# Optimization experiments

Measured on AMD Instinct MI355X. Metric: run time of the kernel, lower is better.

Reference implementation:

```python
import jax, jax.numpy as jnp
import numpy as np

B, T, D, H = 8, 1024, 512, 8
DK = D // H


def setup_inputs() -> dict:
    key = jax.random.key(0)
    ks = jax.random.split(key, 6)
    s = 0.02
    return {
        "inputs": jax.random.normal(ks[0], (B, T, D), jnp.float32),
        "ln1_g": jnp.ones((D,), jnp.float32),
        "ln1_b": jnp.zeros((D,), jnp.float32),
        "ln2_g": jnp.ones((D,), jnp.float32),
        "ln2_b": jnp.zeros((D,), jnp.float32),
        "W_qkv": jax.random.normal(ks[1], (3 * D, D), jnp.float32) * s,
        "W_pos": jax.random.normal(ks[2], (D, D), jnp.float32) * s,
        "W_out": jax.random.normal(ks[3], (D, D), jnp.float32) * s,
        "b_out": jnp.zeros((D,), jnp.float32),
        "pos_bias_u": jax.random.normal(ks[4], (H, DK), jnp.float32) * s,
        "pos_bias_v": jax.random.normal(ks[5], (H, DK), jnp.float32) * s,
    }


def layer_norm(x, g, b, eps=1e-5):
    mu = jnp.mean(x, axis=-1, keepdims=True)
    var = jnp.var(x, axis=-1, keepdims=True)
    return (x - mu) * jax.lax.rsqrt(var + eps) * g + b


def rel_shift(x):
    # x: (b, h, t1, t2); Transformer-XL pad-reshape-slice relative shift
    b, h, t1, t2 = x.shape
    xp = jnp.pad(x, ((0, 0), (0, 0), (0, 0), (1, 0)))  # zero col at front
    xp = xp.reshape(b, h, t2 + 1, t1)[:, :, 1:, :]
    return xp.reshape(b, h, t1, t2)


def reference(inputs, ln1_g, ln1_b, ln2_g, ln2_b, W_qkv, W_pos, W_out, b_out,
              pos_bias_u, pos_bias_v):
    b, t, d = inputs.shape
    # PositionalEmbedding: pos_seq is the literal data values inputs[0,:,0]
    pos_seq = inputs[0, :, 0]
    inv_freq = 1.0 / (10000.0 ** (jnp.arange(0, d, 2, dtype=jnp.float32) / d))
    sin_inp = pos_seq[:, None] * inv_freq[None, :]  # (T, D/2)
    pos_emb = jnp.concatenate([jnp.sin(sin_inp), jnp.cos(sin_inp)], axis=-1)  # (T, D)
    # outer layer norm, then inner layer norm inside forward_qkv
    x = layer_norm(inputs, ln1_g, ln1_b)
    xn = layer_norm(x, ln2_g, ln2_b)
    qkv = xn @ W_qkv.T  # (B, T, 3D)
    q, k, v = jnp.split(qkv, 3, axis=-1)
    q = q.reshape(b, t, H, DK)                       # (B, T, H, DK)
    k = k.reshape(b, t, H, DK).transpose(0, 2, 1, 3)  # (B, H, T, DK)
    v = v.reshape(b, t, H, DK).transpose(0, 2, 1, 3)  # (B, H, T, DK)
    p = (pos_emb @ W_pos.T).reshape(t, H, DK)         # (T, H, DK), pos batch = 1
    qu = (q + pos_bias_u).transpose(0, 2, 1, 3)       # (B, H, T, DK)
    qv = (q + pos_bias_v).transpose(0, 2, 1, 3)
    ac = jnp.einsum('bhqd,bhkd->bhqk', qu, k)
    bd = jnp.einsum('bhqd,khd->bhqk', qv, p)
    bd = rel_shift(bd)
    scores = (ac + bd) / jnp.sqrt(jnp.float32(DK))
    attn = jax.nn.softmax(scores, axis=-1)
    out = jnp.einsum('bhqk,bhkd->bqhd', attn, v).reshape(b, t, d)
    return out @ W_out.T + b_out
```

## Files before the change

kernel.cpp:

```cpp
#include <hip/hip_runtime.h>
#include <stdint.h>

#define B_ 8
#define T_ 1024
#define D_ 512
#define H_ 8
#define DK_ 64
#define M_ (B_*T_)

#define PREP_CAST_BLKS (5 * D_ * D_ / 4 / 256)
#define PREP_POS_BLKS  (T_)
#define PREP_LN_BLKS   (M_)
#define PREP_BLKS      (PREP_CAST_BLKS + PREP_POS_BLKS + PREP_LN_BLKS)

typedef unsigned short u16;
typedef __attribute__((ext_vector_type(8))) short bf16x8;
typedef __attribute__((ext_vector_type(4))) float f32x4;

static __device__ __forceinline__ u16 f2bf(float f) {
  union { float f; unsigned u; } v; v.f = f;
  unsigned r = (v.u + 0x7fffu + ((v.u >> 16) & 1u)) >> 16;
  return (u16)r;
}
static __device__ __forceinline__ u16 f2bf_ru(float f) {
  union { float f; unsigned u; } v; v.f = f;
  return (u16)((v.u + 0x8000u) >> 16);
}
static __device__ __forceinline__ float bf2f(u16 u) {
  union { unsigned u; float f; } v; v.u = ((unsigned)u) << 16;
  return v.f;
}
static __device__ __forceinline__ void async16(const u16* g, u16* l) {
  __builtin_amdgcn_global_load_lds(
      (const __attribute__((address_space(1))) void*)g,
      (__attribute__((address_space(3))) void*)l, 16, 0, 0);
}
static __device__ __forceinline__ f32x4 mfma16(bf16x8 a, bf16x8 b, f32x4 c) {
  return __builtin_amdgcn_mfma_f32_16x16x32_bf16(a, b, c, 0, 0, 0);
}

__global__ __launch_bounds__(256)
void prep_k(const float* __restrict__ wq, const float* __restrict__ wp,
            const float* __restrict__ wo, u16* __restrict__ dq,
            u16* __restrict__ dp, u16* __restrict__ dwo,
            const float* __restrict__ x, u16* __restrict__ pe,
            const float* __restrict__ g1, const float* __restrict__ b1,
            const float* __restrict__ g2, const float* __restrict__ b2,
            u16* __restrict__ xn) {
  __shared__ float red[16];
  const int blk = blockIdx.x;
  const int t = threadIdx.x;
  if (blk < PREP_CAST_BLKS) {
    const int na = 3 * D_ * D_ / 4, nb = D_ * D_ / 4;
    int i = blk * 256 + t;
    const float* s; u16* d; int j;
    if (i < na) { s = wq; d = dq; j = i; }
    else if (i < na + nb) { s = wp; d = dp; j = i - na; }
    else { s = wo; d = dwo; j = i - na - nb; }
    float4 v = ((const float4*)s)[j];
    ushort4 o;
    o.x = f2bf(v.x); o.y = f2bf(v.y); o.z = f2bf(v.z); o.w = f2bf(v.w);
    ((ushort4*)d)[j] = o;
  } else if (blk < PREP_CAST_BLKS + PREP_POS_BLKS) {
    const int tt = blk - PREP_CAST_BLKS;
    float pos = x[(size_t)tt * D_];
    float invf = expf(-(2.f * t / (float)D_) * 9.210340371976184f);
    float ang = pos * invf;
    pe[(size_t)tt * D_ + t] = f2bf(sinf(ang));
    pe[(size_t)tt * D_ + 256 + t] = f2bf(cosf(ang));
  } else {
    const int row = blk - PREP_CAST_BLKS - PREP_POS_BLKS;
    const float2 v = *(const float2*)(x + (size_t)row * D_ + t * 2);
    float a = v.x + v.y;
    float b = v.x * v.x + v.y * v.y;
    for (int off = 32; off; off >>= 1) { a += __shfl_down(a, off, 64); b += __shfl_down(b, off, 64); }
    if ((t & 63) == 0) { red[t >> 6] = a; red[8 + (t >> 6)] = b; }
    __syncthreads();
    a = red[0] + red[1] + red[2] + red[3];
    b = red[8] + red[9] + red[10] + red[11];
    float mu = a * (1.f / D_);
    float var = b * (1.f / D_) - mu * mu;
    float rs = rsqrtf(var + 1e-5f);
    const float2 g1v = *(const float2*)(g1 + t * 2);
    const float2 b1v = *(const float2*)(b1 + t * 2);
    float y0 = (v.x - mu) * rs * g1v.x + b1v.x;
    float y1 = (v.y - mu) * rs * g1v.y + b1v.y;
    __syncthreads();
    a = y0 + y1;
    b = y0 * y0 + y1 * y1;
    for (int off = 32; off; off >>= 1) { a += __shfl_down(a, off, 64); b += __shfl_down(b, off, 64); }
    if ((t & 63) == 0) { red[t >> 6] = a; red[8 + (t >> 6)] = b; }
    __syncthreads();
    a = red[0] + red[1] + red[2] + red[3];
    b = red[8] + red[9] + red[10] + red[11];
    mu = a * (1.f / D_);
    var = b * (1.f / D_) - mu * mu;
    rs = rsqrtf(var + 1e-5f);
    const float2 g2v = *(const float2*)(g2 + t * 2);
    const float2 b2v = *(const float2*)(b2 + t * 2);
    u16* o = xn + (size_t)row * D_ + t * 2;
    o[0] = f2bf((y0 - mu) * rs * g2v.x + b2v.x);
    o[1] = f2bf((y1 - mu) * rs * g2v.y + b2v.y);
  }
}

template<int MODE>
__global__ __launch_bounds__(256, 2)
void gemm_k(const u16* __restrict__ A, const u16* __restrict__ Bw,
            int M, int N, int K,
            u16* __restrict__ o0, u16* __restrict__ o1, u16* __restrict__ o2,
            float* __restrict__ fo, const float* __restrict__ bo) {
  __shared__ u16 As[2][128 * 32];
  __shared__ u16 Bs[2][128 * 32];
  const int tid = threadIdx.x;
  const int l = tid & 63, w = tid >> 6;
  const int m0 = blockIdx.x * 128, n0 = blockIdx.y * 128;
  const int wm = (w >> 1) * 64, wn = (w & 1) * 64;
  const int nk = K >> 5;

  auto stage = [&](int bufi, int kt) {
    const int row = tid >> 2;
    const int cg = ((tid & 3) ^ ((row + (row >> 2)) & 3)) * 8;
    const u16* ga = A + (size_t)(m0 + row) * K + kt * 32 + cg;
    u16* la = &As[bufi][tid * 8];
    async16(ga, la);
    async16(ga + (size_t)64 * K, la + 64 * 32);
    const u16* gb = Bw + (size_t)(n0 + row) * K + kt * 32 + cg;
    u16* lb = &Bs[bufi][tid * 8];
    async16(gb, lb);
    async16(gb + (size_t)64 * K, lb + 64 * 32);
  };

  const int fl = (((l & 15) + ((l & 15) >> 2)) & 3);
  const int coff = ((l >> 4) ^ fl) * 8;
  const int aoff = (l & 15) * 32 + coff;

  f32x4 acc[4][4] = {};
  stage(0, 0);
  for (int kt = 0; kt < nk; ++kt) {
    __syncthreads();
    if (kt + 1 < nk) stage((kt + 1) & 1, kt + 1);
    const u16* as = As[kt & 1];
    const u16* bs = Bs[kt & 1];
    bf16x8 af[4], bfr[4];
#pragma unroll
    for (int i = 0; i < 4; ++i)
      af[i] = *(const bf16x8*)&as[(wm + i * 16) * 32 + aoff];
#pragma unroll
    for (int j = 0; j < 4; ++j)
      bfr[j] = *(const bf16x8*)&bs[(wn + j * 16) * 32 + aoff];
#pragma unroll
    for (int i = 0; i < 4; ++i)
#pragma unroll
      for (int j = 0; j < 4; ++j)
        acc[i][j] = mfma16(af[i], bfr[j], acc[i][j]);
  }

#pragma unroll
  for (int i = 0; i < 4; ++i)
#pragma unroll
    for (int j = 0; j < 4; ++j) {
      const int row0 = m0 + wm + i * 16 + ((l >> 4) << 2);
      const int col = n0 + wn + j * 16 + (l & 15);
      if (MODE == 0) {
        const int sec = col >> 9, cc = col & 511;
        const int hh = cc >> 6, dk = cc & 63;
        const int bb = row0 >> 10, t0r = row0 & 1023;
        if (sec == 2) {
          ushort4 v4;
          v4.x = f2bf(acc[i][j][0]); v4.y = f2bf(acc[i][j][1]);
          v4.z = f2bf(acc[i][j][2]); v4.w = f2bf(acc[i][j][3]);
          *(ushort4*)&o2[((size_t)(bb * H_ + hh) * DK_ + dk) * T_ + t0r] = v4;
        } else {
          u16* dst = (sec == 0) ? o0 : o1;
#pragma unroll
          for (int r = 0; r < 4; ++r)
            dst[((size_t)(bb * H_ + hh) * T_ + t0r + r) * DK_ + dk] = f2bf(acc[i][j][r]);
        }
      } else if (MODE == 1) {
        const int hh = col >> 6, dk = col & 63;
#pragma unroll
        for (int r = 0; r < 4; ++r)
          o0[((size_t)hh * T_ + row0 + r) * DK_ + dk] = f2bf(acc[i][j][r]);
      } else {
#pragma unroll
        for (int r = 0; r < 4; ++r)
          fo[(size_t)(row0 + r) * D_ + col] = acc[i][j][r] + bo[col];
      }
    }
}

__global__ __launch_bounds__(512)
void attn_k(const u16* __restrict__ q, const u16* __restrict__ kb,
            const u16* __restrict__ vt, const u16* __restrict__ pb,
            const float* __restrict__ bu, const float* __restrict__ bv,
            u16* __restrict__ ao) {
  __shared__ u16 k_lds[64 * 64];
  __shared__ u16 v_lds[64 * 64];
  __shared__ u16 pscr[8][16 * 72];

  const int tid = threadIdx.x;
  const int l = tid & 63, w = tid >> 6;
  const int dd = blockIdx.x;
  const int bh = (dd & 7) * 8 + ((dd >> 3) & 7);
  const int qg = dd >> 6;
  const int q0 = qg * 128;
  const int qbA = qg * 2, qbB = qg * 2 + 1;
  const int b = bh >> 3, h = bh & 7;
  const int diagKt = qbA + (w >> 2);

  const u16* qB = q + (size_t)bh * T_ * DK_;
  const u16* kB = kb + (size_t)bh * T_ * DK_;
  const u16* vB = vt + (size_t)bh * DK_ * T_;
  const u16* pB2 = pb + (size_t)h * T_ * DK_ - 65 * DK_;

  const float SCALE = 0.125f * 1.4426950408889634f;

  bf16x8 quf[2], qvf[2], qsf[2];
  {
    const float* buH = bu + h * DK_;
    const float* bvH = bv + h * DK_;
    const int row = q0 + w * 16 + (l & 15);
    const int row2 = (row + 1 < T_) ? row + 1 : T_ - 1;
    const int ko = (l >> 4) * 8;
    const bf16x8 qa0 = *(const bf16x8*)(qB + (size_t)row * DK_ + ko);
    const bf16x8 qa1 = *(const bf16x8*)(qB + (size_t)row * DK_ + ko + 32);
    const bf16x8 qs0 = *(const bf16x8*)(qB + (size_t)row2 * DK_ + ko);
    const bf16x8 qs1 = *(const bf16x8*)(qB + (size_t)row2 * DK_ + ko + 32);
#pragma unroll
    for (int jj = 0; jj < 8; ++jj) {
      float f0 = bf2f((u16)qa0[jj]), f1 = bf2f((u16)qa1[jj]);
      float g0 = bf2f((u16)qs0[jj]), g1 = bf2f((u16)qs1[jj]);
      float u0 = buH[ko + jj], u1 = buH[ko + 32 + jj];
      float v0 = bvH[ko + jj], v1 = bvH[ko + 32 + jj];
      quf[0][jj] = (short)f2bf((f0 + u0) * SCALE);
      quf[1][jj] = (short)f2bf((f1 + u1) * SCALE);
      qvf[0][jj] = (short)f2bf((f0 + v0) * SCALE);
      qvf[1][jj] = (short)f2bf((f1 + v1) * SCALE);
      qsf[0][jj] = (short)f2bf((g0 + v0) * SCALE);
      qsf[1][jj] = (short)f2bf((g1 + v1) * SCALE);
    }
  }

  f32x4 o[4] = {};
  float lrun[4] = {0.f, 0.f, 0.f, 0.f};
  float sv[4][4];

  const int rbase = 112 - w * 16;
  const int rbaseX = 48 - (w & 3) * 16;
  u16* pwv = &pscr[w][0];
  const int lrow = l & 15;
  const int c0s = ((l >> 4) ^ (l & 7)) * 8;
  const int c1s = c0s ^ 32;
  const int qrow0 = (l >> 4) * 4;

  int srcb[4], hi[4];
#pragma unroll
  for (int r = 0; r < 4; ++r) {
    int d = lrow - qrow0 - r + 15;
    srcb[r] = (((l >> 4) * 16 + (d & 15)) << 2);
    hi[r] = d >> 4;
  }

  const int rr = tid >> 3;
  const int cb = (tid & 7) * 8;
  const int swz = ((tid & 7) ^ (rr & 7)) * 8;
  const int wdst = rr * 64 + swz;
  const unsigned kOffE = (unsigned)(rr * DK_ + cb);
  const unsigned vOffE = (unsigned)(rr * T_ + cb);

  uint4 kreg, vreg;
  auto loadK = [&](int t) { kreg = *(const uint4*)(kB + kOffE + (unsigned)(t * 64 * DK_)); };
  auto loadV = [&](int t) { vreg = *(const uint4*)(vB + vOffE + (unsigned)(t * 64)); };
  auto mainJb = [&](int t) {
    return (t <= qbA) ? (T_ - 128 + t * 64 - q0) : (t * 64 - q0 - 129);
  };

  const u16* pwBase = pB2 + (size_t)(65 + rbase + lrow) * DK_ + (l >> 4) * 8;
  bf16x8 bp0[5], bp1[5];
  auto loadBand = [&](int jb) {
#pragma unroll
    for (int fu = 0; fu < 5; ++fu) {
      const u16* p = pwBase + (jb + fu * 16) * DK_;
      bp0[fu] = *(const bf16x8*)p;
      bp1[fu] = *(const bf16x8*)(p + 32);
    }
  };

  loadK(0); loadV(0); loadBand(mainJb(0));

  for (int kt = 0; kt < 16; ++kt) {
    const bool transA = (kt == qbA), transB = (kt == qbB);
    const bool mainLower = (kt <= qbA);
    const bool mainMask = mainLower ? (kt == diagKt) : (kt <= diagKt + 1);
    const bool myExtra = (transA && w < 4) || (transB && w >= 4);
    const int k0 = kt * 64;

    __syncthreads();
    *(uint4*)&k_lds[wdst] = kreg;
    *(uint4*)&v_lds[wdst] = vreg;
    asm volatile("s_waitcnt lgkmcnt(0)" ::: "memory");
    __builtin_amdgcn_sched_barrier(0);
    __builtin_amdgcn_s_barrier();
    __builtin_amdgcn_sched_barrier(0);

    if (kt < 15) { loadK(kt + 1); loadV(kt + 1); }

    {
      __builtin_amdgcn_s_setprio(1);
#pragma unroll
      for (int nf = 0; nf < 4; ++nf) {
        const u16* kb0 = &k_lds[(nf * 16 + lrow) * 64];
        bf16x8 b0 = *(const bf16x8*)(kb0 + c0s);
        bf16x8 b1 = *(const bf16x8*)(kb0 + c1s);
        f32x4 acs = {};
        acs = mfma16(quf[0], b0, acs);
        acs = mfma16(quf[1], b1, acs);
#pragma unroll
        for (int r = 0; r < 4; ++r) sv[nf][r] = acs[r];
      }
      __builtin_amdgcn_s_setprio(0);
    }

    {
      bf16x8 A0, A1;
      if (mainLower) { A0 = qvf[0]; A1 = qvf[1]; } else { A0 = qsf[0]; A1 = qsf[1]; }
      f32x4 c[5];
      __builtin_amdgcn_s_setprio(1);
#pragma unroll
      for (int fu = 0; fu < 5; ++fu) {
        f32x4 cc = {};
        cc = mfma16(A0, bp0[fu], cc);
        cc = mfma16(A1, bp1[fu], cc);
        c[fu] = cc;
      }
      __builtin_amdgcn_s_setprio(0);
      if (kt < 15) loadBand(mainJb(kt + 1));
#pragma unroll
      for (int r = 0; r < 4; ++r) {
        float rot[5];
#pragma unroll
        for (int fu = 0; fu < 5; ++fu)
          rot[fu] = __int_as_float(
              __builtin_amdgcn_ds_bpermute(srcb[r], __float_as_int(c[fu][r])));
#pragma unroll
        for (int nf = 0; nf < 4; ++nf) {
          float bd = hi[r] ? rot[nf + 1] : rot[nf];
          if (mainMask) {
            int rel = (k0 + nf * 16 + lrow) - (q0 + w * 16 + qrow0 + r);
            bool ok = mainLower ? (rel <= 0) : (rel >= 2);
            bd = ok ? bd : 0.f;
          }
          sv[nf][r] += bd;
        }
      }
    }

    if (myExtra) {
      bf16x8 A0, A1;
      if (w < 4) { A0 = qsf[0]; A1 = qsf[1]; } else { A0 = qvf[0]; A1 = qvf[1]; }
      const int jbx = (w < 4) ? -65 : (T_ - 64);
      const u16* pxBase = pB2 + (size_t)(65 + jbx + rbaseX + lrow) * DK_ + (l >> 4) * 8;
      f32x4 c[5];
      __builtin_amdgcn_s_setprio(1);
#pragma unroll
      for (int fu = 0; fu < 5; ++fu) {
        const u16* p = pxBase + fu * 16 * DK_;
        bf16x8 p0 = *(const bf16x8*)p;
        bf16x8 p1 = *(const bf16x8*)(p + 32);
        f32x4 cc = {};
        cc = mfma16(A0, p0, cc);
        cc = mfma16(A1, p1, cc);
        c[fu] = cc;
      }
      __builtin_amdgcn_s_setprio(0);
#pragma unroll
      for (int r = 0; r < 4; ++r) {
        float rot[5];
#pragma unroll
        for (int fu = 0; fu < 5; ++fu)
          rot[fu] = __int_as_float(
              __builtin_amdgcn_ds_bpermute(srcb[r], __float_as_int(c[fu][r])));
#pragma unroll
        for (int nf = 0; nf < 4; ++nf) {
          float bd = hi[r] ? rot[nf + 1] : rot[nf];
          int rel = (k0 + nf * 16 + lrow) - (q0 + w * 16 + qrow0 + r);
          bool ok = (w < 4) ? (rel >= 2) : (rel <= 0);
          sv[nf][r] += ok ? bd : 0.f;
        }
      }
    }

    {
#pragma unroll
      for (int nf = 0; nf < 4; ++nf)
#pragma unroll
        for (int r = 0; r < 4; ++r)
          sv[nf][r] = __builtin_amdgcn_exp2f(sv[nf][r]);
#pragma unroll
      for (int r = 0; r < 4; ++r)
        lrun[r] += (sv[0][r] + sv[1][r]) + (sv[2][r] + sv[3][r]);

#pragma unroll
      for (int nf = 0; nf < 4; ++nf)
#pragma unroll
        for (int r = 0; r < 4; ++r)
          pwv[(qrow0 + r) * 72 + nf * 16 + lrow] = f2bf_ru(sv[nf][r]);

      bf16x8 pa0 = *(const bf16x8*)&pwv[lrow * 72 + (l >> 4) * 8];
      bf16x8 pa1 = *(const bf16x8*)&pwv[lrow * 72 + 32 + (l >> 4) * 8];
      __builtin_amdgcn_s_setprio(1);
#pragma unroll
      for (int df = 0; df < 4; ++df) {
        const u16* vb2 = &v_lds[(df * 16 + lrow) * 64];
        bf16x8 v0 = *(const bf16x8*)(vb2 + c0s);
        bf16x8 v1 = *(const bf16x8*)(vb2 + c1s);
        o[df] = mfma16(pa0, v0, o[df]);
        o[df] = mfma16(pa1, v1, o[df]);
      }
      __builtin_amdgcn_s_setprio(0);
    }
  }

#pragma unroll
  for (int r = 0; r < 4; ++r) {
#pragma unroll
    for (int off = 1; off < 16; off <<= 1) lrun[r] += __shfl_xor(lrun[r], off, 64);
    lrun[r] = 1.f / lrun[r];
  }
#pragma unroll
  for (int df = 0; df < 4; ++df)
#pragma unroll
    for (int r = 0; r < 4; ++r) {
      int qq = q0 + w * 16 + (l >> 4) * 4 + r;
      int dk = df * 16 + (l & 15);
      float val = o[df][r] * lrun[r];
      ao[((size_t)b * T_ + qq) * D_ + h * DK_ + dk] = f2bf(val);
    }
}

extern "C" void kernel_launch(void* const* d_in, const int* in_sizes, int n_in,
                              void* d_out, int out_size, void* d_ws, size_t ws_size,
                              hipStream_t stream) {
  const float* inputs = (const float*)d_in[0];
  const float* ln1_g = (const float*)d_in[1];
  const float* ln1_b = (const float*)d_in[2];
  const float* ln2_g = (const float*)d_in[3];
  const float* ln2_b = (const float*)d_in[4];
  const float* W_qkv = (const float*)d_in[5];
  const float* W_pos = (const float*)d_in[6];
  const float* W_out = (const float*)d_in[7];
  const float* b_out = (const float*)d_in[8];
  const float* pbu = (const float*)d_in[9];
  const float* pbv = (const float*)d_in[10];
  float* out = (float*)d_out;

  char* ws = (char*)d_ws;
  size_t off = 0;
  auto alloc = [&](size_t bytes) {
    char* p = ws + off;
    off += (bytes + 255) & ~(size_t)255;
    return p;
  };
  u16* xn   = (u16*)alloc((size_t)M_ * D_ * 2);
  u16* wqkv = (u16*)alloc((size_t)3 * D_ * D_ * 2);
  u16* wpos = (u16*)alloc((size_t)D_ * D_ * 2);
  u16* wout = (u16*)alloc((size_t)D_ * D_ * 2);
  u16* pemb = (u16*)alloc((size_t)T_ * D_ * 2);
  u16* qB   = (u16*)alloc((size_t)M_ * D_ * 2);
  u16* kbB  = (u16*)alloc((size_t)M_ * D_ * 2);
  u16* vtB  = (u16*)alloc((size_t)M_ * D_ * 2);
  u16* pbuf = (u16*)alloc((size_t)H_ * T_ * DK_ * 2);
  u16* aoB  = (u16*)alloc((size_t)M_ * D_ * 2);
  if (ws_size < off) return;

  prep_k<<<PREP_BLKS, 256, 0, stream>>>(W_qkv, W_pos, W_out, wqkv, wpos, wout,
                                        inputs, pemb, ln1_g, ln1_b, ln2_g, ln2_b, xn);
  gemm_k<1><<<dim3(T_ / 128, D_ / 128), 256, 0, stream>>>(
      pemb, wpos, T_, D_, D_, pbuf, nullptr, nullptr, nullptr, nullptr);
  gemm_k<0><<<dim3(M_ / 128, (3 * D_) / 128), 256, 0, stream>>>(
      xn, wqkv, M_, 3 * D_, D_, qB, kbB, vtB, nullptr, nullptr);
  attn_k<<<512, 512, 0, stream>>>(qB, kbB, vtB, pbuf, pbu, pbv, aoB);
  gemm_k<2><<<dim3(M_ / 128, D_ / 128), 256, 0, stream>>>(
      aoB, wout, M_, D_, D_, nullptr, nullptr, nullptr, out, b_out);
}
```

Measured before the change: 155.0 us.

## Give each attention wave two query tiles and stage positional bands in LDS

Halves the attention block to 4 waves, each now handling two 16-row query groups, so every K, V and positional-band fragment read from LDS is reused by two MFMA groups. The positional band and the cross-diagonal extra band are loaded cooperatively into new LDS buffers with async global-to-LDS copies, replacing per-wave global loads held in registers. The register prefetch of the next K/V tile is removed: each iteration now issues its copies and waits on vmcnt(0) before computing, so global latency is no longer overlapped with compute. LDS use grows to roughly 65KB per block, which may limit how many blocks fit on a CU.

```diff
diff --git a/kernel.cpp b/kernel.cpp
--- a/kernel.cpp
+++ b/kernel.cpp
@@ -190,14 +190,16 @@
     }
 }
 
-__global__ __launch_bounds__(512)
+__global__ __launch_bounds__(256)
 void attn_k(const u16* __restrict__ q, const u16* __restrict__ kb,
             const u16* __restrict__ vt, const u16* __restrict__ pb,
             const float* __restrict__ bu, const float* __restrict__ bv,
             u16* __restrict__ ao) {
   __shared__ u16 k_lds[64 * 64];
   __shared__ u16 v_lds[64 * 64];
-  __shared__ u16 pscr[8][16 * 72];
+  __shared__ u16 pm_lds[192 * 64];
+  __shared__ u16 px_lds[128 * 64];
+  __shared__ u16 pscr[4][16 * 72];
 
   const int tid = threadIdx.x;
   const int l = tid & 63, w = tid >> 6;
@@ -207,7 +209,6 @@
   const int q0 = qg * 128;
   const int qbA = qg * 2, qbB = qg * 2 + 1;
   const int b = bh >> 3, h = bh & 7;
-  const int diagKt = qbA + (w >> 2);
 
   const u16* qB = q + (size_t)bh * T_ * DK_;
   const u16* kB = kb + (size_t)bh * T_ * DK_;
@@ -216,11 +217,13 @@
 
   const float SCALE = 0.125f * 1.4426950408889634f;
 
-  bf16x8 quf[2], qvf[2], qsf[2];
-  {
+  bf16x8 quf[2][2], qvf[2][2], qsf[2][2];
+#pragma unroll
+  for (int g = 0; g < 2; ++g) {
+    const int gg = 2 * w + g;
     const float* buH = bu + h * DK_;
     const float* bvH = bv + h * DK_;
-    const int row = q0 + w * 16 + (l & 15);
+    const int row = q0 + gg * 16 + (l & 15);
     const int row2 = (row + 1 < T_) ? row + 1 : T_ - 1;
     const int ko = (l >> 4) * 8;
     const bf16x8 qa0 = *(const bf16x8*)(qB + (size_t)row * DK_ + ko);
@@ -233,21 +236,21 @@
       float g0 = bf2f((u16)qs0[jj]), g1 = bf2f((u16)qs1[jj]);
       float u0 = buH[ko + jj], u1 = buH[ko + 32 + jj];
       float v0 = bvH[ko + jj], v1 = bvH[ko + 32 + jj];
-      quf[0][jj] = (short)f2bf((f0 + u0) * SCALE);
-      quf[1][jj] = (short)f2bf((f1 + u1) * SCALE);
-      qvf[0][jj] = (short)f2bf((f0 + v0) * SCALE);
-      qvf[1][jj] = (short)f2bf((f1 + v1) * SCALE);
-      qsf[0][jj] = (short)f2bf((g0 + v0) * SCALE);
-      qsf[1][jj] = (short)f2bf((g1 + v1) * SCALE);
+      quf[g][0][jj] = (short)f2bf((f0 + u0) * SCALE);
+      quf[g][1][jj] = (short)f2bf((f1 + u1) * SCALE);
+      qvf[g][0][jj] = (short)f2bf((f0 + v0) * SCALE);
+      qvf[g][1][jj] = (short)f2bf((f1 + v1) * SCALE);
+      qsf[g][0][jj] = (short)f2bf((g0 + v0) * SCALE);
+      qsf[g][1][jj] = (short)f2bf((g1 + v1) * SCALE);
     }
   }
 
-  f32x4 o[4] = {};
-  float lrun[4] = {0.f, 0.f, 0.f, 0.f};
-  float sv[4][4];
-
-  const int rbase = 112 - w * 16;
-  const int rbaseX = 48 - (w & 3) * 16;
+  f32x4 o[2][4] = {};
+  float lrun[2][4] = {};
+  float sv[2][4][4];
+
+  const int rbU = 96 - 32 * w;
+  const int rbXU = 32 - 32 * (w & 1);
   u16* pwv = &pscr[w][0];
   const int lrow = l & 15;
   const int c0s = ((l >> 4) ^ (l & 7)) * 8;
@@ -262,181 +265,211 @@
     hi[r] = d >> 4;
   }
 
-  const int rr = tid >> 3;
-  const int cb = (tid & 7) * 8;
-  const int swz = ((tid & 7) ^ (rr & 7)) * 8;
-  const int wdst = rr * 64 + swz;
-  const unsigned kOffE = (unsigned)(rr * DK_ + cb);
-  const unsigned vOffE = (unsigned)(rr * T_ + cb);
-
-  uint4 kreg, vreg;
-  auto loadK = [&](int t) { kreg = *(const uint4*)(kB + kOffE + (unsigned)(t * 64 * DK_)); };
-  auto loadV = [&](int t) { vreg = *(const uint4*)(vB + vOffE + (unsigned)(t * 64)); };
-  auto mainJb = [&](int t) {
-    return (t <= qbA) ? (T_ - 128 + t * 64 - q0) : (t * 64 - q0 - 129);
-  };
-
-  const u16* pwBase = pB2 + (size_t)(65 + rbase + lrow) * DK_ + (l >> 4) * 8;
-  bf16x8 bp0[5], bp1[5];
-  auto loadBand = [&](int jb) {
-#pragma unroll
-    for (int fu = 0; fu < 5; ++fu) {
-      const u16* p = pwBase + (jb + fu * 16) * DK_;
-      bp0[fu] = *(const bf16x8*)p;
-      bp1[fu] = *(const bf16x8*)(p + 32);
-    }
-  };
-
-  loadK(0); loadV(0); loadBand(mainJb(0));
+  const int rr0 = tid >> 3;
+  const int cg8 = ((tid & 7) ^ (rr0 & 7)) * 8;
+  const int dst8 = (tid & 7) * 8;
 
   for (int kt = 0; kt < 16; ++kt) {
     const bool transA = (kt == qbA), transB = (kt == qbB);
     const bool mainLower = (kt <= qbA);
-    const bool mainMask = mainLower ? (kt == diagKt) : (kt <= diagKt + 1);
-    const bool myExtra = (transA && w < 4) || (transB && w >= 4);
     const int k0 = kt * 64;
+    const int jb = mainLower ? (T_ - 128 + k0 - q0) : (k0 - q0 - 129);
 
     __syncthreads();
-    *(uint4*)&k_lds[wdst] = kreg;
-    *(uint4*)&v_lds[wdst] = vreg;
-    asm volatile("s_waitcnt lgkmcnt(0)" ::: "memory");
+    {
+      const u16* gk = kB + (size_t)(k0 + rr0) * DK_ + cg8;
+      async16(gk, &k_lds[rr0 * 64 + dst8]);
+      async16(gk + 32 * DK_, &k_lds[(rr0 + 32) * 64 + dst8]);
+      const u16* gv = vB + (size_t)rr0 * T_ + k0 + cg8;
+      async16(gv, &v_lds[rr0 * 64 + dst8]);
+      async16(gv + 32 * T_, &v_lds[(rr0 + 32) * 64 + dst8]);
+      const u16* gp = pB2 + (size_t)(jb + 65 + rr0) * DK_ + cg8;
+#pragma unroll
+      for (int i = 0; i < 6; ++i)
+        async16(gp + (size_t)(i * 32) * DK_, &pm_lds[(rr0 + i * 32) * 64 + dst8]);
+      if (transA || transB) {
+        const int jbx = transA ? -65 : (T_ - 64);
+        const u16* gx = pB2 + (size_t)(jbx + 65 + rr0) * DK_ + cg8;
+#pragma unroll
+        for (int i = 0; i < 4; ++i)
+          async16(gx + (size_t)(i * 32) * DK_, &px_lds[(rr0 + i * 32) * 64 + dst8]);
+      }
+    }
+    asm volatile("s_waitcnt vmcnt(0)" ::: "memory");
     __builtin_amdgcn_sched_barrier(0);
     __builtin_amdgcn_s_barrier();
     __builtin_amdgcn_sched_barrier(0);
 
-    if (kt < 15) { loadK(kt + 1); loadV(kt + 1); }
-
     {
-      __builtin_amdgcn_s_setprio(1);
+      bf16x8 kfA[4], kfB[4];
 #pragma unroll
       for (int nf = 0; nf < 4; ++nf) {
         const u16* kb0 = &k_lds[(nf * 16 + lrow) * 64];
-        bf16x8 b0 = *(const bf16x8*)(kb0 + c0s);
-        bf16x8 b1 = *(const bf16x8*)(kb0 + c1s);
-        f32x4 acs = {};
-        acs = mfma16(quf[0], b0, acs);
-        acs = mfma16(quf[1], b1, acs);
-#pragma unroll
-        for (int r = 0; r < 4; ++r) sv[nf][r] = acs[r];
-      }
+        kfA[nf] = *(const bf16x8*)(kb0 + c0s);
+        kfB[nf] = *(const bf16x8*)(kb0 + c1s);
+      }
+      __builtin_amdgcn_s_setprio(1);
+#pragma unroll
+      for (int g = 0; g < 2; ++g)
+#pragma unroll
+        for (int nf = 0; nf < 4; ++nf) {
+          f32x4 acs = {};
+          acs = mfma16(quf[g][0], kfA[nf], acs);
+          acs = mfma16(quf[g][1], kfB[nf], acs);
+#pragma unroll
+          for (int r = 0; r < 4; ++r) sv[g][nf][r] = acs[r];
+        }
       __builtin_amdgcn_s_setprio(0);
     }
 
     {
-      bf16x8 A0, A1;
-      if (mainLower) { A0 = qvf[0]; A1 = qvf[1]; } else { A0 = qsf[0]; A1 = qsf[1]; }
-      f32x4 c[5];
-      __builtin_amdgcn_s_setprio(1);
-#pragma unroll
-      for (int fu = 0; fu < 5; ++fu) {
-        f32x4 cc = {};
-        cc = mfma16(A0, bp0[fu], cc);
-        cc = mfma16(A1, bp1[fu], cc);
-        c[fu] = cc;
-      }
-      __builtin_amdgcn_s_setprio(0);
-      if (kt < 15) loadBand(mainJb(kt + 1));
-#pragma unroll
-      for (int r = 0; r < 4; ++r) {
-        float rot[5];
-#pragma unroll
-        for (int fu = 0; fu < 5; ++fu)
-          rot[fu] = __int_as_float(
-              __builtin_amdgcn_ds_bpermute(srcb[r], __float_as_int(c[fu][r])));
-#pragma unroll
-        for (int nf = 0; nf < 4; ++nf) {
-          float bd = hi[r] ? rot[nf + 1] : rot[nf];
-          if (mainMask) {
-            int rel = (k0 + nf * 16 + lrow) - (q0 + w * 16 + qrow0 + r);
-            bool ok = mainLower ? (rel <= 0) : (rel >= 2);
-            bd = ok ? bd : 0.f;
+      bf16x8 wfA[6], wfB[6];
+#pragma unroll
+      for (int j = 0; j < 6; ++j) {
+        const u16* pb0 = &pm_lds[(rbU + j * 16 + lrow) * 64];
+        wfA[j] = *(const bf16x8*)(pb0 + c0s);
+        wfB[j] = *(const bf16x8*)(pb0 + c1s);
+      }
+#pragma unroll
+      for (int g = 0; g < 2; ++g) {
+        const int gg = 2 * w + g;
+        bf16x8 A0 = mainLower ? qvf[g][0] : qsf[g][0];
+        bf16x8 A1 = mainLower ? qvf[g][1] : qsf[g][1];
+        f32x4 c[5];
+        __builtin_amdgcn_s_setprio(1);
+#pragma unroll
+        for (int fu = 0; fu < 5; ++fu) {
+          f32x4 cc = {};
+          cc = mfma16(A0, wfA[fu + 1 - g], cc);
+          cc = mfma16(A1, wfB[fu + 1 - g], cc);
+          c[fu] = cc;
+        }
+        __builtin_amdgcn_s_setprio(0);
+        const int diag = qbA + (gg >> 2);
+        const bool msk = mainLower ? (kt == diag) : (kt <= diag + 1);
+        const int qbase = q0 + gg * 16;
+#pragma unroll
+        for (int r = 0; r < 4; ++r) {
+          float rot[5];
+#pragma unroll
+          for (int fu = 0; fu < 5; ++fu)
+            rot[fu] = __int_as_float(
+                __builtin_amdgcn_ds_bpermute(srcb[r], __float_as_int(c[fu][r])));
+#pragma unroll
+          for (int nf = 0; nf < 4; ++nf) {
+            float bd = hi[r] ? rot[nf + 1] : rot[nf];
+            if (msk) {
+              int rel = (k0 + nf * 16 + lrow) - (qbase + qrow0 + r);
+              bool ok = mainLower ? (rel <= 0) : (rel >= 2);
+              bd = ok ? bd : 0.f;
+            }
+            sv[g][nf][r] += bd;
           }
-          sv[nf][r] += bd;
-        }
-      }
-    }
-
-    if (myExtra) {
-      bf16x8 A0, A1;
-      if (w < 4) { A0 = qsf[0]; A1 = qsf[1]; } else { A0 = qvf[0]; A1 = qvf[1]; }
-      const int jbx = (w < 4) ? -65 : (T_ - 64);
-      const u16* pxBase = pB2 + (size_t)(65 + jbx + rbaseX + lrow) * DK_ + (l >> 4) * 8;
-      f32x4 c[5];
-      __builtin_amdgcn_s_setprio(1);
-#pragma unroll
-      for (int fu = 0; fu < 5; ++fu) {
-        const u16* p = pxBase + fu * 16 * DK_;
-        bf16x8 p0 = *(const bf16x8*)p;
-        bf16x8 p1 = *(const bf16x8*)(p + 32);
-        f32x4 cc = {};
-        cc = mfma16(A0, p0, cc);
-        cc = mfma16(A1, p1, cc);
-        c[fu] = cc;
-      }
-      __builtin_amdgcn_s_setprio(0);
-#pragma unroll
-      for (int r = 0; r < 4; ++r) {
-        float rot[5];
-#pragma unroll
-        for (int fu = 0; fu < 5; ++fu)
-          rot[fu] = __int_as_float(
-              __builtin_amdgcn_ds_bpermute(srcb[r], __float_as_int(c[fu][r])));
-#pragma unroll
-        for (int nf = 0; nf < 4; ++nf) {
-          float bd = hi[r] ? rot[nf + 1] : rot[nf];
-          int rel = (k0 + nf * 16 + lrow) - (q0 + w * 16 + qrow0 + r);
-          bool ok = (w < 4) ? (rel >= 2) : (rel <= 0);
-          sv[nf][r] += ok ? bd : 0.f;
+        }
+      }
+    }
+
+    if ((transA && w < 2) || (transB && w >= 2)) {
+      const bool upperX = (w < 2);
+      bf16x8 xfA[6], xfB[6];
+#pragma unroll
+      for (int j = 0; j < 6; ++j) {
+        const u16* pb0 = &px_lds[(rbXU + j * 16 + lrow) * 64];
+        xfA[j] = *(const bf16x8*)(pb0 + c0s);
+        xfB[j] = *(const bf16x8*)(pb0 + c1s);
+      }
+#pragma unroll
+      for (int g = 0; g < 2; ++g) {
+        const int gg = 2 * w + g;
+        bf16x8 A0 = upperX ? qsf[g][0] : qvf[g][0];
+        bf16x8 A1 = upperX ? qsf[g][1] : qvf[g][1];
+        f32x4 c[5];
+        __builtin_amdgcn_s_setprio(1);
+#pragma unroll
+        for (int fu = 0; fu < 5; ++fu) {
+          f32x4 cc = {};
+          cc = mfma16(A0, xfA[fu + 1 - g], cc);
+          cc = mfma16(A1, xfB[fu + 1 - g], cc);
+          c[fu] = cc;
+        }
+        __builtin_amdgcn_s_setprio(0);
+        const int qbase = q0 + gg * 16;
+#pragma unroll
+        for (int r = 0; r < 4; ++r) {
+          float rot[5];
+#pragma unroll
+          for (int fu = 0; fu < 5; ++fu)
+            rot[fu] = __int_as_float(
+                __builtin_amdgcn_ds_bpermute(srcb[r], __float_as_int(c[fu][r])));
+#pragma unroll
+          for (int nf = 0; nf < 4; ++nf) {
+            float bd = hi[r] ? rot[nf + 1] : rot[nf];
+            int rel = (k0 + nf * 16 + lrow) - (qbase + qrow0 + r);
+            bool ok = upperX ? (rel >= 2) : (rel <= 0);
+            sv[g][nf][r] += ok ? bd : 0.f;
+          }
         }
       }
     }
 
     {
-#pragma unroll
-      for (int nf = 0; nf < 4; ++nf)
-#pragma unroll
-        for (int r = 0; r < 4; ++r)
-          sv[nf][r] = __builtin_amdgcn_exp2f(sv[nf][r]);
-#pragma unroll
-      for (int r = 0; r < 4; ++r)
-        lrun[r] += (sv[0][r] + sv[1][r]) + (sv[2][r] + sv[3][r]);
-
-#pragma unroll
-      for (int nf = 0; nf < 4; ++nf)
-#pragma unroll
-        for (int r = 0; r < 4; ++r)
-          pwv[(qrow0 + r) * 72 + nf * 16 + lrow] = f2bf_ru(sv[nf][r]);
-
-      bf16x8 pa0 = *(const bf16x8*)&pwv[lrow * 72 + (l >> 4) * 8];
-      bf16x8 pa1 = *(const bf16x8*)&pwv[lrow * 72 + 32 + (l >> 4) * 8];
-      __builtin_amdgcn_s_setprio(1);
+      bf16x8 vfA[4], vfB[4];
 #pragma unroll
       for (int df = 0; df < 4; ++df) {
         const u16* vb2 = &v_lds[(df * 16 + lrow) * 64];
-        bf16x8 v0 = *(const bf16x8*)(vb2 + c0s);
-        bf16x8 v1 = *(const bf16x8*)(vb2 + c1s);
-        o[df] = mfma16(pa0, v0, o[df]);
-        o[df] = mfma16(pa1, v1, o[df]);
-      }
-      __builtin_amdgcn_s_setprio(0);
+        vfA[df] = *(const bf16x8*)(vb2 + c0s);
+        vfB[df] = *(const bf16x8*)(vb2 + c1s);
+      }
+#pragma unroll
+      for (int g = 0; g < 2; ++g) {
+#pragma unroll
+        for (int nf = 0; nf < 4; ++nf)
+#pragma unroll
+          for (int r = 0; r < 4; ++r)
+            sv[g][nf][r] = __builtin_amdgcn_exp2f(sv[g][nf][r]);
+#pragma unroll
+        for (int r = 0; r < 4; ++r)
+          lrun[g][r] += (sv[g][0][r] + sv[g][1][r]) + (sv[g][2][r] + sv[g][3][r]);
+
+#pragma unroll
+        for (int nf = 0; nf < 4; ++nf)
+#pragma unroll
+          for (int r = 0; r < 4; ++r)
+            pwv[(qrow0 + r) * 72 + nf * 16 + lrow] = f2bf_ru(sv[g][nf][r]);
+
+        bf16x8 pa0 = *(const bf16x8*)&pwv[lrow * 72 + (l >> 4) * 8];
+        bf16x8 pa1 = *(const bf16x8*)&pwv[lrow * 72 + 32 + (l >> 4) * 8];
+        __builtin_amdgcn_s_setprio(1);
+#pragma unroll
+        for (int df = 0; df < 4; ++df) {
+          o[g][df] = mfma16(pa0, vfA[df], o[g][df]);
+          o[g][df] = mfma16(pa1, vfB[df], o[g][df]);
+        }
+        __builtin_amdgcn_s_setprio(0);
+      }
     }
   }
 
 #pragma unroll
-  for (int r = 0; r < 4; ++r) {
-#pragma unroll
-    for (int off = 1; off < 16; off <<= 1) lrun[r] += __shfl_xor(lrun[r], off, 64);
-    lrun[r] = 1.f / lrun[r];
+  for (int g = 0; g < 2; ++g) {
+    const int gg = 2 * w + g;
+#pragma unroll
+    for (int r = 0; r < 4; ++r) {
+      float s = lrun[g][r];
+#pragma unroll
+      for (int off = 1; off < 16; off <<= 1) s += __shfl_xor(s, off, 64);
+      lrun[g][r] = 1.f / s;
+    }
+#pragma unroll
+    for (int df = 0; df < 4; ++df)
+#pragma unroll
+      for (int r = 0; r < 4; ++r) {
+        int qq = q0 + gg * 16 + qrow0 + r;
+        int dk = df * 16 + (l & 15);
+        float val = o[g][df][r] * lrun[g][r];
+        ao[((size_t)b * T_ + qq) * D_ + h * DK_ + dk] = f2bf(val);
+      }
   }
-#pragma unroll
-  for (int df = 0; df < 4; ++df)
-#pragma unroll
-    for (int r = 0; r < 4; ++r) {
-      int qq = q0 + w * 16 + (l >> 4) * 4 + r;
-      int dk = df * 16 + (l & 15);
-      float val = o[df][r] * lrun[r];
-      ao[((size_t)b * T_ + qq) * D_ + h * DK_ + dk] = f2bf(val);
-    }
 }
 
 extern "C" void kernel_launch(void* const* d_in, const int* in_sizes, int n_in,
@@ -480,7 +513,7 @@
       pemb, wpos, T_, D_, D_, pbuf, nullptr, nullptr, nullptr, nullptr);
   gemm_k<0><<<dim3(M_ / 128, (3 * D_) / 128), 256, 0, stream>>>(
       xn, wqkv, M_, 3 * D_, D_, qB, kbB, vtB, nullptr, nullptr);
-  attn_k<<<512, 512, 0, stream>>>(qB, kbB, vtB, pbuf, pbu, pbv, aoB);
+  attn_k<<<512, 256, 0, stream>>>(qB, kbB, vtB, pbuf, pbu, pbv, aoB);
   gemm_k<2><<<dim3(M_ / 128, D_ / 128), 256, 0, stream>>>(
       aoB, wout, M_, D_, D_, nullptr, nullptr, nullptr, out, b_out);
 }
```

After: 172.0 us. +11.0%, slower.
